# Kernel optimization log

Hardware: AMD Instinct MI355X
Metric: run time of the kernel (lower is better)

Reference implementation:

```python
import jax, jax.numpy as jnp
import numpy as np

BLOCK = 16          # NVFP4 block size along contraction dim
FP4_MAX = 6.0       # max magnitude of E2M1
FP8_MAX = 448.0     # max magnitude of float8_e4m3fn

_LEVELS = jnp.array([0.0, 0.5, 1.0, 1.5, 2.0, 3.0, 4.0, 6.0], dtype=jnp.float32)
_MIDS   = jnp.array([0.25, 0.75, 1.25, 1.75, 2.5, 3.5, 5.0], dtype=jnp.float32)


def quantize_dequant_nvfp4(t, global_scale):
    """Fake-quantize t (last dim % 16 == 0) to NVFP4: per-16-block fp8-e4m3
    scale times global fp32 scale, values snapped to the E2M1 grid."""
    shp = t.shape
    tb = t.reshape(shp[:-1] + (shp[-1] // BLOCK, BLOCK))
    amax = jnp.max(jnp.abs(tb), axis=-1, keepdims=True)
    # per-block scale, quantized to float8_e4m3fn as in TensorCoreNVFP4Layout
    bs = amax / (FP4_MAX * global_scale)
    bs8 = bs.astype(jnp.float8_e4m3fn).astype(jnp.float32)
    scale = bs8 * global_scale                       # effective dequant scale
    v = tb / jnp.maximum(scale, 1e-12)
    sign = jnp.sign(v)
    a = jnp.clip(jnp.abs(v), 0.0, FP4_MAX)
    idx = jnp.sum(a[..., None] > _MIDS, axis=-1)     # nearest E2M1 level
    q = _LEVELS[idx] * sign * scale
    return q.reshape(shp)


def setup_inputs() -> dict:
    key = jax.random.key(0)
    kx, kw, kb = jax.random.split(key, 3)
    x = jax.random.normal(kx, (8192, 4096), dtype=jnp.float32)
    weight = jax.random.normal(kw, (4096, 4096), dtype=jnp.float32) * 0.02
    bias = jax.random.normal(kb, (4096,), dtype=jnp.float32) * 0.02
    # global scales (weight_scale_2 / input_scale): amax / (6 * 448)
    input_scale = jnp.max(jnp.abs(x)) / (FP4_MAX * FP8_MAX)
    weight_scale = jnp.max(jnp.abs(weight)) / (FP4_MAX * FP8_MAX)
    return {"x": x, "weight": weight, "bias": bias,
            "input_scale": input_scale, "weight_scale": weight_scale}


def reference(x, weight, bias, input_scale, weight_scale):
    xq = quantize_dequant_nvfp4(x, input_scale)      # [T, K]
    wq = quantize_dequant_nvfp4(weight, weight_scale)  # [N, K]
    return jnp.einsum('tk,nk->tn', xq, wq) + bias    # F.linear
```

## Files before the change

kernel.cpp:

```cpp
#include <hip/hip_runtime.h>
#include <hip/hip_bf16.h>
#include <stdint.h>

typedef __attribute__((ext_vector_type(8))) __bf16 bf16x8;
typedef __attribute__((ext_vector_type(4))) float f32x4;
typedef __attribute__((ext_vector_type(4))) unsigned int u32x4;

#define BM 256
#define BN 256
#define BKT 32
#define SLOT 16384


__device__ __forceinline__ float fp8_e4m3_rne(float x) {
  if (x < 0.015625f) {
    return rintf(x * 512.0f) * 0.001953125f;
  }
  uint32_t u = __float_as_uint(x);
  uint32_t keep = u & 0xFFF00000u;
  uint32_t rem  = u & 0x000FFFFFu;
  uint32_t lsb  = (u >> 20) & 1u;
  if (rem > 0x80000u || (rem == 0x80000u && lsb)) keep += 0x100000u;
  return __uint_as_float(keep);
}

__device__ __forceinline__ float snap_lvl(float a) {
  if (a > 5.0f)  return 6.0f;
  if (a > 3.5f)  return 4.0f;
  if (a > 2.5f)  return 3.0f;
  if (a > 1.75f) return 2.0f;
  if (a > 1.25f) return 1.5f;
  if (a > 0.75f) return 1.0f;
  if (a > 0.25f) return 0.5f;
  return 0.0f;
}

__global__ __launch_bounds__(256) void quant_nvfp4(
    const float* __restrict__ in, unsigned short* __restrict__ out,
    const float* __restrict__ gsp, int nblk) {
  int b = blockIdx.x * 256 + threadIdx.x;
  if (b >= nblk) return;
  float gs = gsp[0];
  const float4* p = reinterpret_cast<const float4*>(in) + (size_t)b * 4;
  float v[16];
#pragma unroll
  for (int i = 0; i < 4; ++i) {
    float4 t4 = p[i];
    v[i * 4 + 0] = t4.x; v[i * 4 + 1] = t4.y;
    v[i * 4 + 2] = t4.z; v[i * 4 + 3] = t4.w;
  }
  float amax = 0.0f;
#pragma unroll
  for (int i = 0; i < 16; ++i) amax = fmaxf(amax, fabsf(v[i]));
  float bs8 = fp8_e4m3_rne(amax / (6.0f * gs));
  float scale = fmaxf(bs8 * gs, 1e-12f);
  unsigned short o[16];
#pragma unroll
  for (int i = 0; i < 16; ++i) {
    float q = v[i] / scale;
    float a = fminf(fabsf(q), 6.0f);
    float val = copysignf(snap_lvl(a) * bs8, q);
    o[i] = (unsigned short)(__float_as_uint(val) >> 16);
  }
  uint4 w0 = make_uint4((uint32_t)o[0] | ((uint32_t)o[1] << 16),
                        (uint32_t)o[2] | ((uint32_t)o[3] << 16),
                        (uint32_t)o[4] | ((uint32_t)o[5] << 16),
                        (uint32_t)o[6] | ((uint32_t)o[7] << 16));
  uint4 w1 = make_uint4((uint32_t)o[8]  | ((uint32_t)o[9]  << 16),
                        (uint32_t)o[10] | ((uint32_t)o[11] << 16),
                        (uint32_t)o[12] | ((uint32_t)o[13] << 16),
                        (uint32_t)o[14] | ((uint32_t)o[15] << 16));
  uint4* op = reinterpret_cast<uint4*>(out + (size_t)b * 16);
  op[0] = w0;
  op[1] = w1;
}


__device__ __forceinline__ void async_lds16(const void* g, void* l) {
  __builtin_amdgcn_global_load_lds((__attribute__((address_space(1))) void*)(g),
                                   (__attribute__((address_space(3))) void*)(l),
                                   16, 0, 0);
}

#define DSR(dst, a) asm volatile("ds_read_b128 %0, %1" : "=v"(dst) : "v"(a))
#define VMC(S) asm volatile("s_waitcnt vmcnt(" S ")" ::: "memory")
#define BCB(x) __builtin_bit_cast(bf16x8, x)

#define MF4(mi, ar) do {                                                       \
    acc[mi][0] = __builtin_amdgcn_mfma_f32_16x16x32_bf16(BCB(ar), BCB(bT0), acc[mi][0], 0, 0, 0); \
    acc[mi][1] = __builtin_amdgcn_mfma_f32_16x16x32_bf16(BCB(ar), BCB(bT1), acc[mi][1], 0, 0, 0); \
    acc[mi][2] = __builtin_amdgcn_mfma_f32_16x16x32_bf16(BCB(ar), BCB(bT2), acc[mi][2], 0, 0, 0); \
    acc[mi][3] = __builtin_amdgcn_mfma_f32_16x16x32_bf16(BCB(ar), BCB(bT3), acc[mi][3], 0, 0, 0); \
  } while (0)

#define SG_A0(T_, SO) async_lds16(pA0 + (size_t)(T_) * BKT, (char*)As + (SO) + lo0)
#define SG_B0(T_, SO) async_lds16(pB0 + (size_t)(T_) * BKT, (char*)Bs + (SO) + lo0)
#define SG_A1(T_, SO) async_lds16(pA1 + (size_t)(T_) * BKT, (char*)As + (SO) + lo1)
#define SG_B1(T_, SO) async_lds16(pB1 + (size_t)(T_) * BKT, (char*)Bs + (SO) + lo1)

#define PH_LO(SOFF, STG, VMS) do {                                             \
    DSR(bT0, adB[0] + (SOFF)); DSR(bT1, adB[1] + (SOFF));                      \
    DSR(bT2, adB[2] + (SOFF)); DSR(bT3, adB[3] + (SOFF));                      \
    DSR(aL0, adA[0] + (SOFF)); DSR(aL1, adA[1] + (SOFF));                      \
    DSR(aL2, adA[2] + (SOFF)); DSR(aL3, adA[3] + (SOFF));                      \
    STG;                                                                       \
    VMS;                                                                       \
    __builtin_amdgcn_sched_barrier(0);                                         \
    __builtin_amdgcn_s_barrier();                                              \
    asm volatile("s_waitcnt lgkmcnt(0)" ::: "memory");                         \
    __builtin_amdgcn_sched_barrier(0);                                         \
    __builtin_amdgcn_s_setprio(1);                                             \
    MF4(0, aL0); MF4(1, aL1); MF4(2, aL2); MF4(3, aL3);                        \
    __builtin_amdgcn_s_setprio(0);                                             \
    __builtin_amdgcn_sched_barrier(0);                                         \
    __builtin_amdgcn_s_barrier();                                              \
  } while (0)

#define PH_HI(SOFF, STG, VMS) do {                                             \
    DSR(aH0, adA[4] + (SOFF)); DSR(aH1, adA[5] + (SOFF));                      \
    DSR(aH2, adA[6] + (SOFF)); DSR(aH3, adA[7] + (SOFF));                      \
    STG;                                                                       \
    VMS;                                                                       \
    __builtin_amdgcn_sched_barrier(0);                                         \
    __builtin_amdgcn_s_barrier();                                              \
    asm volatile("s_waitcnt lgkmcnt(0)" ::: "memory");                         \
    __builtin_amdgcn_sched_barrier(0);                                         \
    __builtin_amdgcn_s_setprio(1);                                             \
    MF4(4, aH0); MF4(5, aH1); MF4(6, aH2); MF4(7, aH3);                        \
    __builtin_amdgcn_s_setprio(0);                                             \
    __builtin_amdgcn_sched_barrier(0);                                         \
    __builtin_amdgcn_s_barrier();                                              \
  } while (0)

__global__ __launch_bounds__(512, 2) void gemm_bt_bf16(
    const unsigned short* __restrict__ A, const unsigned short* __restrict__ B,
    const float* __restrict__ bias, const float* __restrict__ gsx,
    const float* __restrict__ gsw, float* __restrict__ C,
    int M, int N, int K) {
  __shared__ __align__(16) unsigned short As[4 * 8192];
  __shared__ __align__(16) unsigned short Bs[4 * 8192];

  const int t = threadIdx.x;
  const int l = t & 63;
  const int w = t >> 6;
  const int wm = w >> 2, wn = w & 3;

  const int nbn = N / BN;
  const int nwg = (M / BM) * nbn;
  const int cpx = nwg >> 3;
  int bid = blockIdx.x;
  int logical = (bid & 7) * cpx + (bid >> 3);
  const int bm = logical / nbn, bn = logical % nbn;
  const int brow = bm * BM, bcol = bn * BN;

  unsigned int b0 = (unsigned int)t * 16u;
  unsigned int b1 = b0 + 8192u;
  unsigned int bp0 = b0 ^ (((b0 >> 7) & 3u) << 4);
  unsigned int bp1 = b1 ^ (((b1 >> 7) & 3u) << 4);
  const unsigned int lo0 = b0, lo1 = b1;
  const unsigned short* pA0 = A + (size_t)(brow + (bp0 >> 6)) * K + ((bp0 & 63u) >> 1);
  const unsigned short* pA1 = A + (size_t)(brow + (bp1 >> 6)) * K + ((bp1 & 63u) >> 1);
  const unsigned short* pB0 = B + (size_t)(bcol + (bp0 >> 6)) * K + ((bp0 & 63u) >> 1);
  const unsigned short* pB1 = B + (size_t)(bcol + (bp1 >> 6)) * K + ((bp1 & 63u) >> 1);

  const unsigned baseAu = (unsigned)(uintptr_t)(&As[0]);
  const unsigned baseBu = (unsigned)(uintptr_t)(&Bs[0]);
  unsigned int adA[8], adB[4];
#pragma unroll
  for (int mi = 0; mi < 8; ++mi) {
    unsigned int r = wm * 128 + mi * 16 + (l & 15);
    unsigned int q = r * 64 + ((l >> 4) << 4);
    adA[mi] = baseAu + (q ^ (((q >> 7) & 3u) << 4));
  }
#pragma unroll
  for (int ni = 0; ni < 4; ++ni) {
    unsigned int r = wn * 64 + ni * 16 + (l & 15);
    unsigned int q = r * 64 + ((l >> 4) << 4);
    adB[ni] = baseBu + (q ^ (((q >> 7) & 3u) << 4));
  }

  f32x4 acc[8][4] = {};
  u32x4 aL0, aL1, aL2, aL3, aH0, aH1, aH2, aH3, bT0, bT1, bT2, bT3;

  SG_A0(0, 0);        SG_B0(0, 0);        SG_A1(0, 0);        SG_B1(0, 0);
  SG_A0(1, SLOT);     SG_B0(1, SLOT);     SG_A1(1, SLOT);     SG_B1(1, SLOT);
  SG_A0(2, 2 * SLOT); SG_B0(2, 2 * SLOT); SG_A1(2, 2 * SLOT); SG_B1(2, 2 * SLOT);
  VMC("8");
  __builtin_amdgcn_s_barrier();

#pragma unroll 1
  for (int i = 0; i < 62; ++i) {
    const int base = (i & 1) * 2;
    const int s0 = base * SLOT;
    const int s1 = s0 + SLOT;
    const int sX = (base ^ 3) * SLOT;
    const int sY = s0;
    const int X = 2 * i + 3, Y = 2 * i + 4;
    PH_LO(s0, { SG_A0(X, sX); SG_B0(X, sX); }, (void)0);
    PH_HI(s0, { SG_A1(X, sX); SG_B1(X, sX); }, VMC("8"));
    PH_LO(s1, { SG_A0(Y, sY); SG_B0(Y, sY); }, (void)0);
    PH_HI(s1, { SG_A1(Y, sY); SG_B1(Y, sY); }, VMC("8"));
  }
  PH_LO(0, { SG_A0(127, 3 * SLOT); SG_B0(127, 3 * SLOT); }, (void)0);
  PH_HI(0, { SG_A1(127, 3 * SLOT); SG_B1(127, 3 * SLOT); }, VMC("8"));
  PH_LO(SLOT, {}, (void)0);
  PH_HI(SLOT, {}, VMC("4"));
  PH_LO(2 * SLOT, {}, VMC("0"));
  PH_HI(2 * SLOT, {}, (void)0);
  PH_LO(3 * SLOT, {}, (void)0);
  PH_HI(3 * SLOT, {}, (void)0);

  const float gscale = gsx[0] * gsw[0];
  float bias_r[4];
#pragma unroll
  for (int ni = 0; ni < 4; ++ni)
    bias_r[ni] = bias[bcol + wn * 64 + ni * 16 + (l & 15)];
#pragma unroll
  for (int mi = 0; mi < 8; ++mi) {
#pragma unroll
    for (int ni = 0; ni < 4; ++ni) {
#pragma unroll
      for (int r = 0; r < 4; ++r) {
        int row = brow + wm * 128 + mi * 16 + (l >> 4) * 4 + r;
        int col = bcol + wn * 64 + ni * 16 + (l & 15);
        C[(size_t)row * N + col] = acc[mi][ni][r] * gscale + bias_r[ni];
      }
    }
  }
}


extern "C" void kernel_launch(void* const* d_in, const int* in_sizes, int n_in,
                              void* d_out, int out_size, void* d_ws, size_t ws_size,
                              hipStream_t stream) {
  const float* x    = (const float*)d_in[0];
  const float* wgt  = (const float*)d_in[1];
  const float* bias = (const float*)d_in[2];
  const float* isc  = (const float*)d_in[3];
  const float* wsc  = (const float*)d_in[4];
  float* out = (float*)d_out;

  const int N = in_sizes[2];
  const int K = in_sizes[1] / N;
  const int M = in_sizes[0] / K;

  unsigned short* Aq = (unsigned short*)d_ws;
  unsigned short* Bq = Aq + (size_t)M * K;

  int nblkA = M * K / 16;
  quant_nvfp4<<<(nblkA + 255) / 256, 256, 0, stream>>>(x, Aq, isc, nblkA);
  int nblkB = N * K / 16;
  quant_nvfp4<<<(nblkB + 255) / 256, 256, 0, stream>>>(wgt, Bq, wsc, nblkB);

  dim3 grid((M / BM) * (N / BN));
  gemm_bt_bf16<<<grid, 512, 0, stream>>>(Aq, Bq, bias, isc, wsc, out, M, N, K);
}
```

Before: 291.7 us.

## Fuse the two quantize launches and restage the GEMM pipeline as a 4-slot ring

Merges the activation and weight quantization into one launch that routes each thread to the right tensor, saving a kernel launch and a tail. The GEMM main loop becomes a 4-slot rotation where A tiles are staged in the first phase and B tiles in the second, instead of the earlier half-A/half-B split. LDS reads now go through C++ pointer dereferences rather than inline ds_read asm. The sched_barriers are removed, so the compiler may reorder loads around the MFMAs. This risks different register pressure or weaker overlap between loads and MFMAs.

```diff
diff --git a/kernel.cpp b/kernel.cpp
--- a/kernel.cpp
+++ b/kernel.cpp
@@ -4,7 +4,6 @@
 
 typedef __attribute__((ext_vector_type(8))) __bf16 bf16x8;
 typedef __attribute__((ext_vector_type(4))) float f32x4;
-typedef __attribute__((ext_vector_type(4))) unsigned int u32x4;
 
 #define BM 256
 #define BN 256
@@ -35,17 +34,20 @@
   return 0.0f;
 }
 
-__global__ __launch_bounds__(256) void quant_nvfp4(
-    const float* __restrict__ in, unsigned short* __restrict__ out,
-    const float* __restrict__ gsp, int nblk) {
+__global__ __launch_bounds__(256) void quant_nvfp4_fused(
+    const float* __restrict__ inA, unsigned short* __restrict__ outA,
+    const float* __restrict__ gsA,
+    const float* __restrict__ inB, unsigned short* __restrict__ outB,
+    const float* __restrict__ gsB, int nblkA, int nblkTot) {
   int b = blockIdx.x * 256 + threadIdx.x;
-  if (b >= nblk) return;
-  float gs = gsp[0];
-  const float4* p = reinterpret_cast<const float4*>(in) + (size_t)b * 4;
+  if (b >= nblkTot) return;
+  const float* in; unsigned short* out; float gs;
+  if (b < nblkA) { in = inA + (size_t)b * 16; out = outA + (size_t)b * 16; gs = gsA[0]; }
+  else { int b2 = b - nblkA; in = inB + (size_t)b2 * 16; out = outB + (size_t)b2 * 16; gs = gsB[0]; }
   float v[16];
 #pragma unroll
   for (int i = 0; i < 4; ++i) {
-    float4 t4 = p[i];
+    float4 t4 = reinterpret_cast<const float4*>(in)[i];
     v[i * 4 + 0] = t4.x; v[i * 4 + 1] = t4.y;
     v[i * 4 + 2] = t4.z; v[i * 4 + 3] = t4.w;
   }
@@ -70,7 +72,7 @@
                         (uint32_t)o[10] | ((uint32_t)o[11] << 16),
                         (uint32_t)o[12] | ((uint32_t)o[13] << 16),
                         (uint32_t)o[14] | ((uint32_t)o[15] << 16));
-  uint4* op = reinterpret_cast<uint4*>(out + (size_t)b * 16);
+  uint4* op = reinterpret_cast<uint4*>(out);
   op[0] = w0;
   op[1] = w1;
 }
@@ -82,54 +84,52 @@
                                    16, 0, 0);
 }
 
-#define DSR(dst, a) asm volatile("ds_read_b128 %0, %1" : "=v"(dst) : "v"(a))
 #define VMC(S) asm volatile("s_waitcnt vmcnt(" S ")" ::: "memory")
-#define BCB(x) __builtin_bit_cast(bf16x8, x)
-
-#define MF4(mi, ar) do {                                                       \
-    acc[mi][0] = __builtin_amdgcn_mfma_f32_16x16x32_bf16(BCB(ar), BCB(bT0), acc[mi][0], 0, 0, 0); \
-    acc[mi][1] = __builtin_amdgcn_mfma_f32_16x16x32_bf16(BCB(ar), BCB(bT1), acc[mi][1], 0, 0, 0); \
-    acc[mi][2] = __builtin_amdgcn_mfma_f32_16x16x32_bf16(BCB(ar), BCB(bT2), acc[mi][2], 0, 0, 0); \
-    acc[mi][3] = __builtin_amdgcn_mfma_f32_16x16x32_bf16(BCB(ar), BCB(bT3), acc[mi][3], 0, 0, 0); \
-  } while (0)
-
-#define SG_A0(T_, SO) async_lds16(pA0 + (size_t)(T_) * BKT, (char*)As + (SO) + lo0)
-#define SG_B0(T_, SO) async_lds16(pB0 + (size_t)(T_) * BKT, (char*)Bs + (SO) + lo0)
-#define SG_A1(T_, SO) async_lds16(pA1 + (size_t)(T_) * BKT, (char*)As + (SO) + lo1)
-#define SG_B1(T_, SO) async_lds16(pB1 + (size_t)(T_) * BKT, (char*)Bs + (SO) + lo1)
-
-#define PH_LO(SOFF, STG, VMS) do {                                             \
-    DSR(bT0, adB[0] + (SOFF)); DSR(bT1, adB[1] + (SOFF));                      \
-    DSR(bT2, adB[2] + (SOFF)); DSR(bT3, adB[3] + (SOFF));                      \
-    DSR(aL0, adA[0] + (SOFF)); DSR(aL1, adA[1] + (SOFF));                      \
-    DSR(aL2, adA[2] + (SOFF)); DSR(aL3, adA[3] + (SOFF));                      \
+
+#define LDB(ni, SOFF) (*(const bf16x8*)((const char*)Bs + offB[ni] + (SOFF)))
+#define LDA(mi, SOFF) (*(const bf16x8*)((const char*)As + offA[mi] + (SOFF)))
+
+#define MFMA_ROW(mi, av) do {                                                  \
+    acc[mi][0] = __builtin_amdgcn_mfma_f32_16x16x32_bf16(av, b0f, acc[mi][0], 0, 0, 0); \
+    acc[mi][1] = __builtin_amdgcn_mfma_f32_16x16x32_bf16(av, b1f, acc[mi][1], 0, 0, 0); \
+    acc[mi][2] = __builtin_amdgcn_mfma_f32_16x16x32_bf16(av, b2f, acc[mi][2], 0, 0, 0); \
+    acc[mi][3] = __builtin_amdgcn_mfma_f32_16x16x32_bf16(av, b3f, acc[mi][3], 0, 0, 0); \
+  } while (0)
+
+#define PH1(SOFF, STG) do {                                                    \
+    b0f = LDB(0, SOFF); b1f = LDB(1, SOFF);                                    \
+    b2f = LDB(2, SOFF); b3f = LDB(3, SOFF);                                    \
+    bf16x8 a0f = LDA(0, SOFF), a1f = LDA(1, SOFF);                             \
+    bf16x8 a2f = LDA(2, SOFF), a3f = LDA(3, SOFF);                             \
+    STG;                                                                       \
+    __builtin_amdgcn_s_barrier();                                              \
+    asm volatile("s_waitcnt lgkmcnt(0)" ::: "memory");                         \
+    __builtin_amdgcn_s_setprio(1);                                             \
+    MFMA_ROW(0, a0f); MFMA_ROW(1, a1f); MFMA_ROW(2, a2f); MFMA_ROW(3, a3f);    \
+    __builtin_amdgcn_s_setprio(0);                                             \
+    __builtin_amdgcn_s_barrier();                                              \
+  } while (0)
+
+#define PH2(SOFF, STG, VMS) do {                                               \
+    bf16x8 a4f = LDA(4, SOFF), a5f = LDA(5, SOFF);                             \
+    bf16x8 a6f = LDA(6, SOFF), a7f = LDA(7, SOFF);                             \
     STG;                                                                       \
     VMS;                                                                       \
-    __builtin_amdgcn_sched_barrier(0);                                         \
     __builtin_amdgcn_s_barrier();                                              \
     asm volatile("s_waitcnt lgkmcnt(0)" ::: "memory");                         \
-    __builtin_amdgcn_sched_barrier(0);                                         \
     __builtin_amdgcn_s_setprio(1);                                             \
-    MF4(0, aL0); MF4(1, aL1); MF4(2, aL2); MF4(3, aL3);                        \
+    MFMA_ROW(4, a4f); MFMA_ROW(5, a5f); MFMA_ROW(6, a6f); MFMA_ROW(7, a7f);    \
     __builtin_amdgcn_s_setprio(0);                                             \
-    __builtin_amdgcn_sched_barrier(0);                                         \
-    __builtin_amdgcn_s_barrier();                                              \
-  } while (0)
-
-#define PH_HI(SOFF, STG, VMS) do {                                             \
-    DSR(aH0, adA[4] + (SOFF)); DSR(aH1, adA[5] + (SOFF));                      \
-    DSR(aH2, adA[6] + (SOFF)); DSR(aH3, adA[7] + (SOFF));                      \
-    STG;                                                                       \
-    VMS;                                                                       \
-    __builtin_amdgcn_sched_barrier(0);                                         \
-    __builtin_amdgcn_s_barrier();                                              \
-    asm volatile("s_waitcnt lgkmcnt(0)" ::: "memory");                         \
-    __builtin_amdgcn_sched_barrier(0);                                         \
-    __builtin_amdgcn_s_setprio(1);                                             \
-    MF4(4, aH0); MF4(5, aH1); MF4(6, aH2); MF4(7, aH3);                        \
-    __builtin_amdgcn_s_setprio(0);                                             \
-    __builtin_amdgcn_sched_barrier(0);                                         \
-    __builtin_amdgcn_s_barrier();                                              \
+    __builtin_amdgcn_s_barrier();                                              \
+  } while (0)
+
+#define STG_A(TOFF, SO) do {                                                   \
+    async_lds16(pA0 + (TOFF) * BKT, (char*)As + (SO) + lo0);                   \
+    async_lds16(pA1 + (TOFF) * BKT, (char*)As + (SO) + lo1);                   \
+  } while (0)
+#define STG_B(TOFF, SO) do {                                                   \
+    async_lds16(pB0 + (TOFF) * BKT, (char*)Bs + (SO) + lo0);                   \
+    async_lds16(pB1 + (TOFF) * BKT, (char*)Bs + (SO) + lo1);                   \
   } while (0)
 
 __global__ __launch_bounds__(512, 2) void gemm_bt_bf16(
@@ -163,52 +163,49 @@
   const unsigned short* pB0 = B + (size_t)(bcol + (bp0 >> 6)) * K + ((bp0 & 63u) >> 1);
   const unsigned short* pB1 = B + (size_t)(bcol + (bp1 >> 6)) * K + ((bp1 & 63u) >> 1);
 
-  const unsigned baseAu = (unsigned)(uintptr_t)(&As[0]);
-  const unsigned baseBu = (unsigned)(uintptr_t)(&Bs[0]);
-  unsigned int adA[8], adB[4];
+  unsigned int offA[8], offB[4];
 #pragma unroll
   for (int mi = 0; mi < 8; ++mi) {
     unsigned int r = wm * 128 + mi * 16 + (l & 15);
     unsigned int q = r * 64 + ((l >> 4) << 4);
-    adA[mi] = baseAu + (q ^ (((q >> 7) & 3u) << 4));
+    offA[mi] = q ^ (((q >> 7) & 3u) << 4);
   }
 #pragma unroll
   for (int ni = 0; ni < 4; ++ni) {
     unsigned int r = wn * 64 + ni * 16 + (l & 15);
     unsigned int q = r * 64 + ((l >> 4) << 4);
-    adB[ni] = baseBu + (q ^ (((q >> 7) & 3u) << 4));
+    offB[ni] = q ^ (((q >> 7) & 3u) << 4);
   }
 
   f32x4 acc[8][4] = {};
-  u32x4 aL0, aL1, aL2, aL3, aH0, aH1, aH2, aH3, bT0, bT1, bT2, bT3;
-
-  SG_A0(0, 0);        SG_B0(0, 0);        SG_A1(0, 0);        SG_B1(0, 0);
-  SG_A0(1, SLOT);     SG_B0(1, SLOT);     SG_A1(1, SLOT);     SG_B1(1, SLOT);
-  SG_A0(2, 2 * SLOT); SG_B0(2, 2 * SLOT); SG_A1(2, 2 * SLOT); SG_B1(2, 2 * SLOT);
+  bf16x8 b0f, b1f, b2f, b3f;
+
+  STG_A(0, 0);        STG_B(0, 0);
+  STG_A(1, SLOT);     STG_B(1, SLOT);
+  STG_A(2, 2 * SLOT); STG_B(2, 2 * SLOT);
   VMC("8");
   __builtin_amdgcn_s_barrier();
 
 #pragma unroll 1
-  for (int i = 0; i < 62; ++i) {
-    const int base = (i & 1) * 2;
-    const int s0 = base * SLOT;
-    const int s1 = s0 + SLOT;
-    const int sX = (base ^ 3) * SLOT;
-    const int sY = s0;
-    const int X = 2 * i + 3, Y = 2 * i + 4;
-    PH_LO(s0, { SG_A0(X, sX); SG_B0(X, sX); }, (void)0);
-    PH_HI(s0, { SG_A1(X, sX); SG_B1(X, sX); }, VMC("8"));
-    PH_LO(s1, { SG_A0(Y, sY); SG_B0(Y, sY); }, (void)0);
-    PH_HI(s1, { SG_A1(Y, sY); SG_B1(Y, sY); }, VMC("8"));
-  }
-  PH_LO(0, { SG_A0(127, 3 * SLOT); SG_B0(127, 3 * SLOT); }, (void)0);
-  PH_HI(0, { SG_A1(127, 3 * SLOT); SG_B1(127, 3 * SLOT); }, VMC("8"));
-  PH_LO(SLOT, {}, (void)0);
-  PH_HI(SLOT, {}, VMC("4"));
-  PH_LO(2 * SLOT, {}, VMC("0"));
-  PH_HI(2 * SLOT, {}, (void)0);
-  PH_LO(3 * SLOT, {}, (void)0);
-  PH_HI(3 * SLOT, {}, (void)0);
+  for (int it = 0; it < 31; ++it) {
+    PH1(0,        STG_A(3, 3 * SLOT));
+    PH2(0,        STG_B(3, 3 * SLOT), VMC("8"));
+    PH1(SLOT,     STG_A(4, 0));
+    PH2(SLOT,     STG_B(4, 0), VMC("8"));
+    PH1(2 * SLOT, STG_A(5, SLOT));
+    PH2(2 * SLOT, STG_B(5, SLOT), VMC("8"));
+    PH1(3 * SLOT, STG_A(6, 2 * SLOT));
+    PH2(3 * SLOT, STG_B(6, 2 * SLOT), VMC("8"));
+    pA0 += 4 * BKT; pA1 += 4 * BKT; pB0 += 4 * BKT; pB1 += 4 * BKT;
+  }
+  PH1(0,        STG_A(3, 3 * SLOT));
+  PH2(0,        STG_B(3, 3 * SLOT), VMC("8"));
+  PH1(SLOT,     );
+  PH2(SLOT,     , VMC("4"));
+  PH1(2 * SLOT, );
+  PH2(2 * SLOT, , VMC("0"));
+  PH1(3 * SLOT, );
+  PH2(3 * SLOT, , );
 
   const float gscale = gsx[0] * gsw[0];
   float bias_r[4];
@@ -248,9 +245,10 @@
   unsigned short* Bq = Aq + (size_t)M * K;
 
   int nblkA = M * K / 16;
-  quant_nvfp4<<<(nblkA + 255) / 256, 256, 0, stream>>>(x, Aq, isc, nblkA);
   int nblkB = N * K / 16;
-  quant_nvfp4<<<(nblkB + 255) / 256, 256, 0, stream>>>(wgt, Bq, wsc, nblkB);
+  int nblkTot = nblkA + nblkB;
+  quant_nvfp4_fused<<<(nblkTot + 255) / 256, 256, 0, stream>>>(
+      x, Aq, isc, wgt, Bq, wsc, nblkA, nblkTot);
 
   dim3 grid((M / BM) * (N / BN));
   gemm_bt_bf16<<<grid, 512, 0, stream>>>(Aq, Bq, bias, isc, wsc, out, M, N, K);
```

Measured after the change: 284.1 us. 1.03x faster.
